# Optimization experiments

Measured on AMD Instinct MI355X. Metric: run time of the kernel, lower is better.

The kernel has to match this reference:

```python
import jax, jax.numpy as jnp
import numpy as np


def setup_inputs() -> dict:
    key = jax.random.key(0)
    ks = jax.random.split(key, 8)
    B, T, S, E, H = 8, 1024, 1024, 768, 768
    scale = 1.0 / np.sqrt(E)
    return {
        "x": jax.random.normal(ks[0], (B, T, E), dtype=jnp.float32),
        "encoder_out": jax.random.normal(ks[1], (B, S, E), dtype=jnp.float32),
        "Wq": jax.random.normal(ks[2], (E, H), dtype=jnp.float32) * scale,
        "bq": jnp.zeros((H,), dtype=jnp.float32),
        "Wk": jax.random.normal(ks[3], (E, H), dtype=jnp.float32) * scale,
        "bk": jnp.zeros((H,), dtype=jnp.float32),
        "Wv": jax.random.normal(ks[4], (E, H), dtype=jnp.float32) * scale,
        "bv": jnp.zeros((H,), dtype=jnp.float32),
        "Wp": jax.random.normal(ks[5], (H, E), dtype=jnp.float32) * (1.0 / np.sqrt(H)),
        "bp": jnp.zeros((E,), dtype=jnp.float32),
    }


def reference(x, encoder_out, Wq, bq, Wk, bk, Wv, bv, Wp, bp):
    # Single-head cross-attention: q from x, k/v from encoder_out.
    q = x @ Wq + bq                    # [B,T,H]
    k = encoder_out @ Wk + bk          # [B,S,H]
    v = encoder_out @ Wv + bv          # [B,S,H]
    H = q.shape[-1]
    scores = jnp.einsum("bth,bsh->bts", q, k) * (H ** -0.5)  # [B,T,S]
    attn = jax.nn.softmax(scores, axis=-1)
    # dropout is identity in eval mode
    out = jnp.einsum("bts,bsh->bth", attn, v)                # [B,T,H]
    return out @ Wp + bp                                     # [B,T,E]
```

## Files before the change

kernel.cpp:

```cpp
#include <hip/hip_runtime.h>


typedef __bf16 bf16x8 __attribute__((ext_vector_type(8)));
typedef float  f32x4  __attribute__((ext_vector_type(4)));

__device__ __forceinline__ unsigned short f2bf(float f) {
    unsigned int u = __float_as_uint(f);
    u += 0x7fffu + ((u >> 16) & 1u);
    return (unsigned short)(u >> 16);
}

__device__ __forceinline__ void async_copy16(const void* g, void* s) {
    __builtin_amdgcn_global_load_lds(
        (const __attribute__((address_space(1))) void*)g,
        (__attribute__((address_space(3))) void*)s, 16, 0, 0);
}

__device__ __forceinline__ void gemm_core(
    const unsigned short* __restrict__ Ag,
    const unsigned short* __restrict__ Bg,
    const int K,
    float* __restrict__ Cf, unsigned short* __restrict__ Cb,
    const long ldc, const int transC, const float* __restrict__ bias,
    const float scale, const long row0, const long col0)
{
    __shared__ __align__(16) unsigned short As[8192];
    __shared__ __align__(16) unsigned short Bs[8192];

    const int tid  = threadIdx.x;
    const int lane = tid & 63;
    const int quad = lane >> 4;
    const int l16  = lane & 15;
    const int wv   = tid >> 6;
    const int wm   = (wv >> 1) * 64;
    const int wn   = (wv & 1) * 64;

    const int j8 = ((lane & 7) ^ ((lane >> 3) & 7)) * 8;
    const int rb = wv * 32 + (lane >> 3);
    const unsigned short* sa_src = Ag + (long)rb * K + j8;
    const unsigned short* sb_src = Bg + (long)rb * K + j8;
    const int dbase = (wv * 256 + lane) * 8;

    f32x4 acc[4][4];
#pragma unroll
    for (int i = 0; i < 4; ++i)
#pragma unroll
        for (int j = 0; j < 4; ++j)
            acc[i][j] = f32x4{0.f, 0.f, 0.f, 0.f};

    auto stage = [&](int k0) {
#pragma unroll
        for (int h = 0; h < 4; ++h) {
            async_copy16(sa_src + (long)(h * 8) * K + k0, &As[dbase + h * 512]);
            async_copy16(sb_src + (long)(h * 8) * K + k0, &Bs[dbase + h * 512]);
        }
    };

    auto compute = [&]() {
#pragma unroll
        for (int h = 0; h < 2; ++h) {
            bf16x8 af[4], bf[4];
            const int sl = ((quad + h * 4) ^ (l16 & 7)) * 8;
#pragma unroll
            for (int i = 0; i < 4; ++i) {
                af[i] = *(const bf16x8*)&As[(wm + i * 16 + l16) * 64 + sl];
                bf[i] = *(const bf16x8*)&Bs[(wn + i * 16 + l16) * 64 + sl];
            }
#pragma unroll
            for (int i = 0; i < 4; ++i)
#pragma unroll
                for (int j = 0; j < 4; ++j)
                    acc[i][j] = __builtin_amdgcn_mfma_f32_16x16x32_bf16(
                        af[i], bf[j], acc[i][j], 0, 0, 0);
        }
    };

    const int nk = K >> 6;
    stage(0);
#pragma unroll 1
    for (int t = 0; t < nk; ++t) {
        __syncthreads();
        compute();
        __syncthreads();
        if (t + 1 < nk) stage((t + 1) << 6);
    }

#pragma unroll
    for (int i = 0; i < 4; ++i) {
#pragma unroll
        for (int j = 0; j < 4; ++j) {
            const long r0 = row0 + wm + i * 16 + quad * 4;
            const long c  = col0 + wn + j * 16 + l16;
            const float bb = bias ? bias[c] : 0.0f;
#pragma unroll
            for (int r = 0; r < 4; ++r) {
                const float v = acc[i][j][r] * scale + bb;
                const long rr = r0 + r;
                if (Cb) {
                    if (transC) {
                        Cb[((rr >> 10) * 768 + c) * 1024 + (rr & 1023)] = f2bf(v);
                    } else {
                        Cb[rr * ldc + c] = f2bf(v);
                    }
                } else {
                    Cf[rr * ldc + c] = v;
                }
            }
        }
    }
}


__global__ __launch_bounds__(256, 4) void proj_qkv(
    const unsigned short* __restrict__ xb, const unsigned short* __restrict__ eb,
    const unsigned short* __restrict__ wqt, const unsigned short* __restrict__ wkt,
    const unsigned short* __restrict__ wvt,
    const float* __restrict__ bq, const float* __restrict__ bk,
    const float* __restrict__ bv,
    unsigned short* __restrict__ q, unsigned short* __restrict__ k,
    unsigned short* __restrict__ vt)
{
    const unsigned short *A, *Bt; const float* bias; unsigned short* C;
    int trans = 0;
    switch (blockIdx.z) {
        case 0:  A = xb; Bt = wqt; bias = bq; C = q;  break;
        case 1:  A = eb; Bt = wkt; bias = bk; C = k;  break;
        default: A = eb; Bt = wvt; bias = bv; C = vt; trans = 1; break;
    }
    const int p = blockIdx.x;
    const int g = p & 7, m = p >> 3;
    const long row0 = (long)(g * 8 + (m & 7)) * 128;
    const long col0 = (long)(m >> 3) * 128;
    gemm_core(A + row0 * 768, Bt + col0 * 768, 768,
              nullptr, C, 768, trans, bias, 1.0f, row0, col0);
}

__global__ __launch_bounds__(256, 4) void scores_gemm(
    const unsigned short* __restrict__ q, const unsigned short* __restrict__ k,
    float* __restrict__ sc, float scale)
{
    const int p = blockIdx.x;
    const long b = p & 7;
    const int m  = p >> 3;
    const long row0 = (long)(m & 7) * 128;
    const long col0 = (long)(m >> 3) * 128;
    gemm_core(q + (b * 1024 + row0) * 768, k + b * 786432 + col0 * 768, 768,
              sc + b * 1048576, nullptr, 1024, 0, nullptr, scale, row0, col0);
}

__global__ __launch_bounds__(256, 4) void pv_gemm(
    const unsigned short* __restrict__ p_, const unsigned short* __restrict__ vt,
    unsigned short* __restrict__ ao)
{
    const int p = blockIdx.x;
    const long b = p & 7;
    const int m  = p >> 3;
    const long row0 = (long)(m & 7) * 128;
    const long col0 = (long)(m >> 3) * 128;
    gemm_core(p_ + (b * 1024 + row0) * 1024, vt + b * 786432 + col0 * 1024, 1024,
              nullptr, ao + b * 786432, 768, 0, nullptr, 1.0f, row0, col0);
}

__global__ __launch_bounds__(256, 4) void outproj_gemm(
    const unsigned short* __restrict__ ao, const unsigned short* __restrict__ wpt,
    float* __restrict__ out, const float* __restrict__ bp)
{
    const int p = blockIdx.x;
    const int g = p & 7, m = p >> 3;
    const long row0 = (long)(g * 8 + (m & 7)) * 128;
    const long col0 = (long)(m >> 3) * 128;
    gemm_core(ao + row0 * 768, wpt + col0 * 768, 768,
              out, nullptr, 768, 0, bp, 1.0f, row0, col0);
}


__global__ __launch_bounds__(256) void prep(
    const float* __restrict__ x, const float* __restrict__ enc,
    unsigned short* __restrict__ xb, unsigned short* __restrict__ eb,
    const float* __restrict__ w0, const float* __restrict__ w1,
    const float* __restrict__ w2, const float* __restrict__ w3,
    unsigned short* __restrict__ o0, unsigned short* __restrict__ o1,
    unsigned short* __restrict__ o2, unsigned short* __restrict__ o3)
{
    __shared__ float t[32][33];
    const int bx = blockIdx.x;
    if (bx < 12288) {
        const int i = bx * 256 + threadIdx.x;
        const bool second = (i >= 1572864);
        const int idx = second ? i - 1572864 : i;
        const float4 v = second ? ((const float4*)enc)[idx] : ((const float4*)x)[idx];
        ushort4 o;
        o.x = f2bf(v.x); o.y = f2bf(v.y); o.z = f2bf(v.z); o.w = f2bf(v.w);
        if (second) ((ushort4*)eb)[idx] = o;
        else        ((ushort4*)xb)[idx] = o;
        return;
    }
    const int z  = bx - 12288;
    const int wi = z / 576;
    const int tt = z % 576;
    const float* w; unsigned short* o;
    switch (wi) {
        case 0:  w = w0; o = o0; break;
        case 1:  w = w1; o = o1; break;
        case 2:  w = w2; o = o2; break;
        default: w = w3; o = o3; break;
    }
    const int tx = threadIdx.x & 31;
    const int ty = threadIdx.x >> 5;
    const int k0 = (tt % 24) * 32;
    const int n0 = (tt / 24) * 32;
#pragma unroll
    for (int i = 0; i < 4; ++i)
        t[ty + i * 8][tx] = w[(long)(k0 + ty + i * 8) * 768 + n0 + tx];
    __syncthreads();
#pragma unroll
    for (int i = 0; i < 4; ++i)
        o[(long)(n0 + ty + i * 8) * 768 + k0 + tx] = f2bf(t[tx][ty + i * 8]);
}

__global__ __launch_bounds__(256) void softmax_rows(
    const float* __restrict__ S, unsigned short* __restrict__ P)
{
    const long row = blockIdx.x;
    const float* s = S + row * 1024;
    unsigned short* p = P + row * 1024;
    const int tid  = threadIdx.x;
    const int lane = tid & 63;
    const int wave = tid >> 6;

    float4 v = ((const float4*)s)[tid];
    float m = fmaxf(fmaxf(v.x, v.y), fmaxf(v.z, v.w));
#pragma unroll
    for (int off = 32; off > 0; off >>= 1)
        m = fmaxf(m, __shfl_xor(m, off));
    __shared__ float redm[4], reds[4];
    if (lane == 0) redm[wave] = m;
    __syncthreads();
    m = fmaxf(fmaxf(redm[0], redm[1]), fmaxf(redm[2], redm[3]));

    const float e0 = __expf(v.x - m), e1 = __expf(v.y - m);
    const float e2 = __expf(v.z - m), e3 = __expf(v.w - m);
    float sum = e0 + e1 + e2 + e3;
#pragma unroll
    for (int off = 32; off > 0; off >>= 1)
        sum += __shfl_xor(sum, off);
    if (lane == 0) reds[wave] = sum;
    __syncthreads();
    const float inv = 1.0f / (reds[0] + reds[1] + reds[2] + reds[3]);

    ushort4 o;
    o.x = f2bf(e0 * inv); o.y = f2bf(e1 * inv);
    o.z = f2bf(e2 * inv); o.w = f2bf(e3 * inv);
    ((ushort4*)p)[tid] = o;
}


extern "C" void kernel_launch(void* const* d_in, const int* in_sizes, int n_in,
                              void* d_out, int out_size, void* d_ws, size_t ws_size,
                              hipStream_t stream) {
    const float* x   = (const float*)d_in[0];
    const float* enc = (const float*)d_in[1];
    const float* Wq  = (const float*)d_in[2];
    const float* bq  = (const float*)d_in[3];
    const float* Wk  = (const float*)d_in[4];
    const float* bk  = (const float*)d_in[5];
    const float* Wv  = (const float*)d_in[6];
    const float* bv  = (const float*)d_in[7];
    const float* Wp  = (const float*)d_in[8];
    const float* bp  = (const float*)d_in[9];
    float* out = (float*)d_out;

    char* ws = (char*)d_ws;
    unsigned short* xb  = (unsigned short*)(ws + 0);
    unsigned short* eb  = (unsigned short*)(ws + 12582912);
    unsigned short* q   = (unsigned short*)(ws + 25165824);
    unsigned short* k   = (unsigned short*)(ws + 37748736);
    unsigned short* vt  = (unsigned short*)(ws + 50331648);
    unsigned short* wqt = (unsigned short*)(ws + 62914560);
    unsigned short* wkt = (unsigned short*)(ws + 64094208);
    unsigned short* wvt = (unsigned short*)(ws + 65273856);
    unsigned short* wpt = (unsigned short*)(ws + 66453504);
    float*          sc  = (float*)(ws + 67633152);
    unsigned short* p   = (unsigned short*)(ws + 0);
    unsigned short* ao  = (unsigned short*)(ws + 67633152);

    const float scale = 0.03608439182435161f;

    prep<<<14592, 256, 0, stream>>>(x, enc, xb, eb, Wq, Wk, Wv, Wp,
                                    wqt, wkt, wvt, wpt);

    proj_qkv<<<dim3(384, 1, 3), 256, 0, stream>>>(xb, eb, wqt, wkt, wvt,
                                                  bq, bk, bv, q, k, vt);

    scores_gemm<<<dim3(512, 1, 1), 256, 0, stream>>>(q, k, sc, scale);

    softmax_rows<<<8192, 256, 0, stream>>>(sc, p);

    pv_gemm<<<dim3(384, 1, 1), 256, 0, stream>>>(p, vt, ao);

    outproj_gemm<<<dim3(384, 1, 1), 256, 0, stream>>>(ao, wpt, out, bp);
}
```

Before: 234.6 us.

## Double-buffer LDS in GEMM core and add 256-row tile variant for projections

```diff
diff --git a/kernel.cpp b/kernel.cpp
--- a/kernel.cpp
+++ b/kernel.cpp
@@ -3,6 +3,10 @@
 
 typedef __bf16 bf16x8 __attribute__((ext_vector_type(8)));
 typedef float  f32x4  __attribute__((ext_vector_type(4)));
+
+#define WAIT_VM8 __builtin_amdgcn_s_waitcnt(0x0F78)
+#define WAIT_VM0 __builtin_amdgcn_s_waitcnt(0x0F70)
+#define BAR      __builtin_amdgcn_s_barrier()
 
 __device__ __forceinline__ unsigned short f2bf(float f) {
     unsigned int u = __float_as_uint(f);
@@ -24,8 +28,10 @@
     const long ldc, const int transC, const float* __restrict__ bias,
     const float scale, const long row0, const long col0)
 {
-    __shared__ __align__(16) unsigned short As[8192];
-    __shared__ __align__(16) unsigned short Bs[8192];
+    __shared__ __align__(16) unsigned short As0[8192];
+    __shared__ __align__(16) unsigned short As1[8192];
+    __shared__ __align__(16) unsigned short Bs0[8192];
+    __shared__ __align__(16) unsigned short Bs1[8192];
 
     const int tid  = threadIdx.x;
     const int lane = tid & 63;
@@ -48,23 +54,23 @@
         for (int j = 0; j < 4; ++j)
             acc[i][j] = f32x4{0.f, 0.f, 0.f, 0.f};
 
-    auto stage = [&](int k0) {
+    auto stage = [&](unsigned short* dA, unsigned short* dB, int k0) {
 #pragma unroll
         for (int h = 0; h < 4; ++h) {
-            async_copy16(sa_src + (long)(h * 8) * K + k0, &As[dbase + h * 512]);
-            async_copy16(sb_src + (long)(h * 8) * K + k0, &Bs[dbase + h * 512]);
+            async_copy16(sa_src + (long)(h * 8) * K + k0, &dA[dbase + h * 512]);
+            async_copy16(sb_src + (long)(h * 8) * K + k0, &dB[dbase + h * 512]);
         }
     };
 
-    auto compute = [&]() {
+    auto compute = [&](const unsigned short* sA, const unsigned short* sB) {
 #pragma unroll
         for (int h = 0; h < 2; ++h) {
             bf16x8 af[4], bf[4];
             const int sl = ((quad + h * 4) ^ (l16 & 7)) * 8;
 #pragma unroll
             for (int i = 0; i < 4; ++i) {
-                af[i] = *(const bf16x8*)&As[(wm + i * 16 + l16) * 64 + sl];
-                bf[i] = *(const bf16x8*)&Bs[(wn + i * 16 + l16) * 64 + sl];
+                af[i] = *(const bf16x8*)&sA[(wm + i * 16 + l16) * 64 + sl];
+                bf[i] = *(const bf16x8*)&sB[(wn + i * 16 + l16) * 64 + sl];
             }
 #pragma unroll
             for (int i = 0; i < 4; ++i)
@@ -76,14 +82,25 @@
     };
 
     const int nk = K >> 6;
-    stage(0);
-#pragma unroll 1
-    for (int t = 0; t < nk; ++t) {
-        __syncthreads();
-        compute();
-        __syncthreads();
-        if (t + 1 < nk) stage((t + 1) << 6);
-    }
+    stage(As0, Bs0, 0);
+    stage(As1, Bs1, 64);
+    int k0 = 128;
+
+    for (int t = 0; t < nk - 2; t += 2) {
+        WAIT_VM8; BAR;
+        compute(As0, Bs0);
+        BAR;
+        stage(As0, Bs0, k0); k0 += 64;
+
+        WAIT_VM8; BAR;
+        compute(As1, Bs1);
+        BAR;
+        stage(As1, Bs1, k0); k0 += 64;
+    }
+    WAIT_VM8; BAR;
+    compute(As0, Bs0);
+    WAIT_VM0; BAR;
+    compute(As1, Bs1);
 
 #pragma unroll
     for (int i = 0; i < 4; ++i) {
@@ -110,8 +127,102 @@
     }
 }
 
-
-__global__ __launch_bounds__(256, 4) void proj_qkv(
+__device__ __forceinline__ void gemm_core256(
+    const unsigned short* __restrict__ Ag,
+    const unsigned short* __restrict__ Bg,
+    const int K,
+    float* __restrict__ Cf, unsigned short* __restrict__ Cb,
+    const long ldc, const int transC, const float* __restrict__ bias,
+    const float scale, const long row0, const long col0)
+{
+    __shared__ __align__(16) unsigned short As[16384];
+    __shared__ __align__(16) unsigned short Bs[8192];
+
+    const int tid  = threadIdx.x;
+    const int lane = tid & 63;
+    const int quad = lane >> 4;
+    const int l16  = lane & 15;
+    const int wv   = tid >> 6;
+    const int wm   = (wv >> 1) * 64;
+    const int wn   = (wv & 1) * 64;
+
+    const int j8 = ((tid & 7) ^ ((tid >> 3) & 7)) * 8;
+    const unsigned short* a_src = Ag + (long)(tid >> 3) * K + j8;
+    const unsigned short* b_src = Bg + (long)(tid >> 3) * K + j8;
+    const int dofs = tid * 8;
+
+    f32x4 acc[4][4];
+#pragma unroll
+    for (int i = 0; i < 4; ++i)
+#pragma unroll
+        for (int j = 0; j < 4; ++j)
+            acc[i][j] = f32x4{0.f, 0.f, 0.f, 0.f};
+
+    auto stage = [&](int k0) {
+#pragma unroll
+        for (int h = 0; h < 4; ++h)
+            async_copy16(a_src + (long)(h * 64) * K + k0, &As[h * 4096 + dofs]);
+#pragma unroll
+        for (int h = 0; h < 2; ++h)
+            async_copy16(b_src + (long)(h * 64) * K + k0, &Bs[h * 4096 + dofs]);
+    };
+
+    auto compute = [&]() {
+#pragma unroll
+        for (int h = 0; h < 2; ++h) {
+            bf16x8 af[4], bf[4];
+            const int sl = ((quad + h * 4) ^ (l16 & 7)) * 8;
+#pragma unroll
+            for (int i = 0; i < 4; ++i) {
+                af[i] = *(const bf16x8*)&As[(wm + i * 16 + l16) * 64 + sl];
+                bf[i] = *(const bf16x8*)&Bs[(wn + i * 16 + l16) * 64 + sl];
+            }
+#pragma unroll
+            for (int i = 0; i < 4; ++i)
+#pragma unroll
+                for (int j = 0; j < 4; ++j)
+                    acc[i][j] = __builtin_amdgcn_mfma_f32_16x16x32_bf16(
+                        af[i], bf[j], acc[i][j], 0, 0, 0);
+        }
+    };
+
+    const int nk = K >> 6;
+    stage(0);
+#pragma unroll 1
+    for (int t = 0; t < nk; ++t) {
+        __syncthreads();
+        compute();
+        __syncthreads();
+        if (t + 1 < nk) stage((t + 1) << 6);
+    }
+
+#pragma unroll
+    for (int i = 0; i < 4; ++i) {
+#pragma unroll
+        for (int j = 0; j < 4; ++j) {
+            const long r0 = row0 + wm + i * 16 + quad * 4;
+            const long c  = col0 + wn + j * 16 + l16;
+            const float bb = bias ? bias[c] : 0.0f;
+#pragma unroll
+            for (int r = 0; r < 4; ++r) {
+                const float v = acc[i][j][r] * scale + bb;
+                const long rr = r0 + r;
+                if (Cb) {
+                    if (transC) {
+                        Cb[((rr >> 10) * 768 + c) * 1024 + (rr & 1023)] = f2bf(v);
+                    } else {
+                        Cb[rr * ldc + c] = f2bf(v);
+                    }
+                } else {
+                    Cf[rr * ldc + c] = v;
+                }
+            }
+        }
+    }
+}
+
+
+__global__ __launch_bounds__(512, 4) void proj_qkv(
     const unsigned short* __restrict__ xb, const unsigned short* __restrict__ eb,
     const unsigned short* __restrict__ wqt, const unsigned short* __restrict__ wkt,
     const unsigned short* __restrict__ wvt,
@@ -129,13 +240,13 @@
     }
     const int p = blockIdx.x;
     const int g = p & 7, m = p >> 3;
-    const long row0 = (long)(g * 8 + (m & 7)) * 128;
-    const long col0 = (long)(m >> 3) * 128;
-    gemm_core(A + row0 * 768, Bt + col0 * 768, 768,
-              nullptr, C, 768, trans, bias, 1.0f, row0, col0);
-}
-
-__global__ __launch_bounds__(256, 4) void scores_gemm(
+    const long row0 = (long)(g * 4 + (m & 3)) * 256;
+    const long col0 = (long)(m >> 2) * 128;
+    gemm_core256(A + row0 * 768, Bt + col0 * 768, 768,
+                 nullptr, C, 768, trans, bias, 1.0f, row0, col0);
+}
+
+__global__ __launch_bounds__(256, 2) void scores_gemm(
     const unsigned short* __restrict__ q, const unsigned short* __restrict__ k,
     float* __restrict__ sc, float scale)
 {
@@ -148,7 +259,7 @@
               sc + b * 1048576, nullptr, 1024, 0, nullptr, scale, row0, col0);
 }
 
-__global__ __launch_bounds__(256, 4) void pv_gemm(
+__global__ __launch_bounds__(256, 2) void pv_gemm(
     const unsigned short* __restrict__ p_, const unsigned short* __restrict__ vt,
     unsigned short* __restrict__ ao)
 {
@@ -161,16 +272,16 @@
               nullptr, ao + b * 786432, 768, 0, nullptr, 1.0f, row0, col0);
 }
 
-__global__ __launch_bounds__(256, 4) void outproj_gemm(
+__global__ __launch_bounds__(512, 4) void outproj_gemm(
     const unsigned short* __restrict__ ao, const unsigned short* __restrict__ wpt,
     float* __restrict__ out, const float* __restrict__ bp)
 {
     const int p = blockIdx.x;
     const int g = p & 7, m = p >> 3;
-    const long row0 = (long)(g * 8 + (m & 7)) * 128;
-    const long col0 = (long)(m >> 3) * 128;
-    gemm_core(ao + row0 * 768, wpt + col0 * 768, 768,
-              out, nullptr, 768, 0, bp, 1.0f, row0, col0);
+    const long row0 = (long)(g * 4 + (m & 3)) * 256;
+    const long col0 = (long)(m >> 2) * 128;
+    gemm_core256(ao + row0 * 768, wpt + col0 * 768, 768,
+                 out, nullptr, 768, 0, bp, 1.0f, row0, col0);
 }
 
 
@@ -289,7 +400,7 @@
     prep<<<14592, 256, 0, stream>>>(x, enc, xb, eb, Wq, Wk, Wv, Wp,
                                     wqt, wkt, wvt, wpt);
 
-    proj_qkv<<<dim3(384, 1, 3), 256, 0, stream>>>(xb, eb, wqt, wkt, wvt,
+    proj_qkv<<<dim3(192, 1, 3), 512, 0, stream>>>(xb, eb, wqt, wkt, wvt,
                                                   bq, bk, bv, q, k, vt);
 
     scores_gemm<<<dim3(512, 1, 1), 256, 0, stream>>>(q, k, sc, scale);
@@ -298,5 +409,5 @@
 
     pv_gemm<<<dim3(384, 1, 1), 256, 0, stream>>>(p, vt, ao);
 
-    outproj_gemm<<<dim3(384, 1, 1), 256, 0, stream>>>(ao, wpt, out, bp);
-}
+    outproj_gemm<<<dim3(192, 1, 1), 512, 0, stream>>>(ao, wpt, out, bp);
+}
```

Result: no change. 238.7 us (+1.8%).
